# Performance work log

Hardware: AMD Instinct MI355X
Metric: run time of the kernel (lower is better)

Reference implementation:

```python
import jax, jax.numpy as jnp
import numpy as np

E = 1024   # emb_dim
H = 1024   # hidden_size
L = 2      # num_layers
V = 50257  # vocab_size
S = 2048   # encoder input length
T = 2048   # decoder target length


def setup_inputs() -> dict:
    key = jax.random.key(0)
    ks = jax.random.split(key, 16)
    s = 0.02  # init scale
    f32 = jnp.float32
    return {
        "inputs": jax.random.randint(ks[0], (1, S), 0, V),
        "outputs": jax.random.randint(ks[1], (1, T), 0, V),
        "sos": 1,
        "enc_emb": jax.random.normal(ks[2], (V, E), f32) * s,
        "dec_emb": jax.random.normal(ks[3], (V, E), f32) * s,
        # Stacked LSTM weights; layer-0 input dim == E == H so layers stack.
        "enc_Wih": jax.random.normal(ks[4], (L, 4 * H, H), f32) * s,
        "enc_Whh": jax.random.normal(ks[5], (L, 4 * H, H), f32) * s,
        "enc_bih": jax.random.normal(ks[6], (L, 4 * H), f32) * s,
        "enc_bhh": jax.random.normal(ks[7], (L, 4 * H), f32) * s,
        "dec_Wih": jax.random.normal(ks[8], (L, 4 * H, H), f32) * s,
        "dec_Whh": jax.random.normal(ks[9], (L, 4 * H, H), f32) * s,
        "dec_bih": jax.random.normal(ks[10], (L, 4 * H), f32) * s,
        "dec_bhh": jax.random.normal(ks[11], (L, 4 * H), f32) * s,
        "lin_W": jax.random.normal(ks[12], (V, H), f32) * s,
        "lin_b": jax.random.normal(ks[13], (V,), f32) * s,
    }


def _run_stack(xs, Wih, Whh, bih, bhh, h0, c0):
    # xs: [S, E]; Wih/Whh: [L, 4H, H]; h0/c0: [L, H]
    # PyTorch LSTM gate order: i, f, g, o.
    h_fin, c_fin = [], []
    for l in range(Wih.shape[0]):
        Wi, Wh, bi, bh = Wih[l], Whh[l], bih[l], bhh[l]

        def step(carry, x, Wi=Wi, Wh=Wh, bi=bi, bh=bh):
            h, c = carry
            g = Wi @ x + bi + Wh @ h + bh           # [4H]
            i, f, gg, o = jnp.split(g, 4)
            c = jax.nn.sigmoid(f) * c + jax.nn.sigmoid(i) * jnp.tanh(gg)
            h = jax.nn.sigmoid(o) * jnp.tanh(c)
            return (h, c), h

        (h, c), xs = jax.lax.scan(step, (h0[l], c0[l]), xs)
        h_fin.append(h)
        c_fin.append(c)
    return xs, jnp.stack(h_fin), jnp.stack(c_fin)


def reference(inputs, outputs, sos, enc_emb, dec_emb,
              enc_Wih, enc_Whh, enc_bih, enc_bhh,
              dec_Wih, dec_Whh, dec_bih, dec_bhh,
              lin_W, lin_b):
    # Encoder over the source sequence (batch == 1, squeezed away).
    x = enc_emb[inputs[0]]                       # [S, E]
    z = jnp.zeros((L, H), dtype=x.dtype)
    _, hN, cN = _run_stack(x, enc_Wih, enc_Whh, enc_bih, enc_bhh, z, z)
    # Full teacher forcing: decoder inputs are [sos, outputs[:, :-1]].
    dec_tokens = jnp.concatenate(
        [jnp.array([sos], dtype=outputs.dtype), outputs[0, :-1]])
    y = dec_emb[dec_tokens]                      # [T, E]
    dec_out, _, _ = _run_stack(y, dec_Wih, dec_Whh, dec_bih, dec_bhh, hN, cN)
    logits = dec_out @ lin_W.T + lin_b           # [T, V]
    return logits
```

## Files before the change

### kernel.cpp

```cpp
#include <hip/hip_runtime.h>
#include <hip/hip_bf16.h>
#include <math.h>

#define S_LEN 2048
#define T_LEN 2048
#define HID   1024
#define GATES 4096
#define VOCAB 50257
#define SPINCAP 262144

typedef unsigned int u32;
typedef unsigned long long ull;
typedef u32 u32x4 __attribute__((ext_vector_type(4)));
typedef float f32x4 __attribute__((ext_vector_type(4)));

__device__ __forceinline__ float fsig_(float x)  { return 1.0f / (1.0f + __expf(-x)); }
__device__ __forceinline__ float ftanh_(float x) { float e = __expf(2.0f * x); return 1.0f - 2.0f / (e + 1.0f); }

__device__ __forceinline__ u32x4 cload16(const ull* p) {
  u32x4 v;
  asm volatile("global_load_dwordx4 %0, %1, off sc0 sc1\n\ts_waitcnt vmcnt(0)"
               : "=v"(v) : "v"(p) : "memory");
  return v;
}

__device__ __forceinline__ u32x4 pollslots(const ull* p, u32 want) {
  u32x4 v = cload16(p);
  int n = 0;
  while (v.y < want || v.w < want) {
    if (++n > SPINCAP) break;
    v = cload16(p);
  }
  return v;
}

__global__ void zero_f4(float4* __restrict__ p, size_t n4) {
  size_t i = (size_t)blockIdx.x * blockDim.x + threadIdx.x;
  size_t stride = (size_t)gridDim.x * blockDim.x;
  for (; i < n4; i += stride) p[i] = make_float4(0.f, 0.f, 0.f, 0.f);
}

__global__ void build_dec_tokens(const int* __restrict__ outputs, const int* __restrict__ sos,
                                 int* __restrict__ toks, int T) {
  int t = blockIdx.x * blockDim.x + threadIdx.x;
  if (t < T) toks[t] = (t == 0) ? sos[0] : outputs[t - 1];
}

__global__ __launch_bounds__(256) void gemm_xwt(
    const float* __restrict__ X, const float* __restrict__ W,
    const float* __restrict__ b1,
    float* __restrict__ C, int M, int N, int K)
{
  __shared__ float Xs[16][68];
  __shared__ float Ws[16][68];
  const int tid = threadIdx.x;
  const int tx = tid & 15;
  const int ty = tid >> 4;
  const int m0 = blockIdx.y * 64;
  const int n0 = blockIdx.x * 64;
  const int lr = tid >> 2;
  const int lc = (tid & 3) * 4;
  float acc[4][4] = {{0.f}};

  for (int k0 = 0; k0 < K; k0 += 16) {
    float4 xv = *(const float4*)(X + (size_t)(m0 + lr) * K + k0 + lc);
    float4 wv = make_float4(0.f, 0.f, 0.f, 0.f);
    int wr = n0 + lr;
    if (wr < N) wv = *(const float4*)(W + (size_t)wr * K + k0 + lc);
    __syncthreads();
    Xs[lc + 0][lr] = xv.x; Xs[lc + 1][lr] = xv.y; Xs[lc + 2][lr] = xv.z; Xs[lc + 3][lr] = xv.w;
    Ws[lc + 0][lr] = wv.x; Ws[lc + 1][lr] = wv.y; Ws[lc + 2][lr] = wv.z; Ws[lc + 3][lr] = wv.w;
    __syncthreads();
#pragma unroll
    for (int kk = 0; kk < 16; ++kk) {
      float4 a = *(const float4*)&Xs[kk][ty * 4];
      float4 b = *(const float4*)&Ws[kk][tx * 4];
      float av[4] = {a.x, a.y, a.z, a.w};
      float bv[4] = {b.x, b.y, b.z, b.w};
#pragma unroll
      for (int i = 0; i < 4; ++i)
#pragma unroll
        for (int j = 0; j < 4; ++j)
          acc[i][j] = fmaf(av[i], bv[j], acc[i][j]);
    }
  }
#pragma unroll
  for (int i = 0; i < 4; ++i) {
    int m = m0 + ty * 4 + i;
#pragma unroll
    for (int j = 0; j < 4; ++j) {
      int n = n0 + tx * 4 + j;
      if (n < N) C[(size_t)m * N + n] = acc[i][j] + (b1 ? b1[n] : 0.f);
    }
  }
}

__global__ __launch_bounds__(512, 1) void lstm2(
    const float* __restrict__ emb,  const int* __restrict__ toks,
    const float* __restrict__ Wi0,  const float* __restrict__ Wh0,
    const float* __restrict__ bi0,  const float* __restrict__ bh0,
    const float* __restrict__ Wi1,  const float* __restrict__ Wh1,
    const float* __restrict__ bi1,  const float* __restrict__ bh1,
    const float* __restrict__ h00,  const float* __restrict__ c00,
    const float* __restrict__ h01,  const float* __restrict__ c01,
    ull* __restrict__ s0, ull* __restrict__ s1,
    float* __restrict__ hf0, float* __restrict__ cf0,
    float* __restrict__ hf1, float* __restrict__ cf1,
    float* __restrict__ dec_out, int T)
{
  const int tid = threadIdx.x;
  const int wg  = blockIdx.x;
  const bool isL0 = (wg < 128);
  const int wgl = isL0 ? wg : wg - 128;

  const int lane16 = tid & 15;
  const int rloc = tid >> 4;
  const int jloc = rloc & 7;
  const int gate = rloc >> 3;
  const int grow = gate * HID + wgl * 8 + jloc;

  __shared__ float lds_x[2][HID];
  __shared__ float lds_h[HID];
  __shared__ float lds_g[32];
  __shared__ float lds_c[8];

  const float* Wi = isL0 ? Wi0 : Wi1;
  const float* Wh = isL0 ? Wh0 : Wh1;
  const float breg = (isL0 ? (bi0[grow] + bh0[grow]) : (bi1[grow] + bh1[grow]));

  f32x4 Wir[16], Whr[16];
  {
    const f32x4* wi = (const f32x4*)(Wi + (size_t)grow * HID);
    const f32x4* wh = (const f32x4*)(Wh + (size_t)grow * HID);
#pragma unroll
    for (int i = 0; i < 16; ++i) {
      Wir[i] = wi[lane16 + i * 16];
      Whr[i] = wh[lane16 + i * 16];
    }
  }
#pragma unroll
  for (int i = 0; i < 16; ++i)
    asm volatile("" : "+v"(Wir[i]), "+v"(Whr[i]));

  {
    const float* hini = isL0 ? h00 : h01;
    const float* cini = isL0 ? c00 : c01;
    if (tid < 8) lds_c[tid] = cini[wgl * 8 + tid];
    if (tid < 256) ((float4*)lds_h)[tid] = ((const float4*)hini)[tid];
    if (isL0 && tid < 256) {
      int tok = toks[0];
      ((float4*)lds_x[0])[tid] = ((const float4*)(emb + (size_t)tok * HID))[tid];
    }
  }
  __syncthreads();

  ull* s_mine = isL0 ? s0 : s1;

  for (int t = 0; t < T; ++t) {
    const int cur = t & 1;

    if (isL0) {
      if (t > 0) {
        const ull* ph = s0 + (size_t)(t - 1) * HID + 2 * tid;
        u32x4 v = pollslots(ph, (u32)t);
        lds_h[2 * tid]     = __uint_as_float(v.x);
        lds_h[2 * tid + 1] = __uint_as_float(v.z);
      }
    } else {
      {
        const ull* px = s0 + (size_t)t * HID + 2 * tid;
        u32x4 v = pollslots(px, (u32)(t + 1));
        lds_x[0][2 * tid]     = __uint_as_float(v.x);
        lds_x[0][2 * tid + 1] = __uint_as_float(v.z);
      }
      if (t > 0) {
        const ull* ph = s1 + (size_t)(t - 1) * HID + 2 * tid;
        u32x4 v = pollslots(ph, (u32)t);
        lds_h[2 * tid]     = __uint_as_float(v.x);
        lds_h[2 * tid + 1] = __uint_as_float(v.z);
      }
    }
    __syncthreads();

    if (isL0 && tid < 256 && t + 1 < T) {
      int tok = toks[t + 1];
      ((float4*)lds_x[cur ^ 1])[tid] = ((const float4*)(emb + (size_t)tok * HID))[tid];
    }

    const float* xbuf = isL0 ? lds_x[cur] : lds_x[0];
    float p0 = 0.f, p1 = 0.f, p2 = 0.f, p3 = 0.f;
#pragma unroll
    for (int i = 0; i < 16; ++i) {
      const float4 xv = *(const float4*)&xbuf[(lane16 << 2) + (i << 6)];
      p0 = fmaf(Wir[i].x, xv.x, p0);
      p1 = fmaf(Wir[i].y, xv.y, p1);
      p2 = fmaf(Wir[i].z, xv.z, p2);
      p3 = fmaf(Wir[i].w, xv.w, p3);
    }
#pragma unroll
    for (int i = 0; i < 16; ++i) {
      const float4 hv = *(const float4*)&lds_h[(lane16 << 2) + (i << 6)];
      p0 = fmaf(Whr[i].x, hv.x, p0);
      p1 = fmaf(Whr[i].y, hv.y, p1);
      p2 = fmaf(Whr[i].z, hv.z, p2);
      p3 = fmaf(Whr[i].w, hv.w, p3);
    }
    float sum = (p0 + p1) + (p2 + p3);
    sum += __shfl_xor(sum, 1);
    sum += __shfl_xor(sum, 2);
    sum += __shfl_xor(sum, 4);
    sum += __shfl_xor(sum, 8);
    if (lane16 == 0) lds_g[rloc] = sum + breg;
    __syncthreads();

    if (tid < 8) {
      const float gi = lds_g[tid];
      const float gf = lds_g[8 + tid];
      const float gg = lds_g[16 + tid];
      const float go = lds_g[24 + tid];
      const float c = fsig_(gf) * lds_c[tid] + fsig_(gi) * ftanh_(gg);
      const float h = fsig_(go) * ftanh_(c);
      lds_c[tid] = c;
      const int col = wgl * 8 + tid;
      const ull pk = ((ull)(u32)(t + 1) << 32) | (ull)__float_as_uint(h);
      __hip_atomic_store(&s_mine[(size_t)t * HID + col], pk,
                         __ATOMIC_RELAXED, __HIP_MEMORY_SCOPE_AGENT);
      if (!isL0 && dec_out) dec_out[(size_t)t * HID + col] = h;
      if (t == T - 1) {
        if (isL0) { if (hf0) hf0[col] = h; if (cf0) cf0[col] = c; }
        else      { if (hf1) hf1[col] = h; if (cf1) cf1[col] = c; }
      }
    }
  }
}

extern "C" void kernel_launch(void* const* d_in, const int* in_sizes, int n_in,
                              void* d_out, int out_size, void* d_ws, size_t ws_size,
                              hipStream_t stream) {
  const int*   inputs  = (const int*)d_in[0];
  const int*   outputs = (const int*)d_in[1];
  const int*   sos     = (const int*)d_in[2];
  const float* enc_emb = (const float*)d_in[3];
  const float* dec_emb = (const float*)d_in[4];
  const float* enc_Wih = (const float*)d_in[5];
  const float* enc_Whh = (const float*)d_in[6];
  const float* enc_bih = (const float*)d_in[7];
  const float* enc_bhh = (const float*)d_in[8];
  const float* dec_Wih = (const float*)d_in[9];
  const float* dec_Whh = (const float*)d_in[10];
  const float* dec_bih = (const float*)d_in[11];
  const float* dec_bhh = (const float*)d_in[12];
  const float* lin_W   = (const float*)d_in[13];
  const float* lin_b   = (const float*)d_in[14];

  float* out = (float*)d_out;
  ull* s0e = (ull*)d_out;
  ull* s1e = s0e + 2097152;
  ull* s0d = s1e + 2097152;
  ull* s1d = s0d + 2097152;

  char* ws = (char*)d_ws;
  float* zerosv = (float*)(ws + 0);
  float* hf0    = (float*)(ws + 4096);
  float* cf0    = (float*)(ws + 8192);
  float* hf1    = (float*)(ws + 12288);
  float* cf1    = (float*)(ws + 16384);
  int*   dtoks  = (int*)(ws + 20480);
  float* B2     = (float*)(ws + ((size_t)1 << 20));

  const size_t WOFF = (size_t)GATES * HID;

  zero_f4<<<2048, 256, 0, stream>>>((float4*)d_out, 4194304);
  zero_f4<<<1, 256, 0, stream>>>((float4*)zerosv, 256);
  build_dec_tokens<<<8, 256, 0, stream>>>(outputs, sos, dtoks, T_LEN);

  lstm2<<<256, 512, 0, stream>>>(
      enc_emb, inputs,
      enc_Wih, enc_Whh, enc_bih, enc_bhh,
      enc_Wih + WOFF, enc_Whh + WOFF, enc_bih + GATES, enc_bhh + GATES,
      zerosv, zerosv, zerosv, zerosv,
      s0e, s1e, hf0, cf0, hf1, cf1, nullptr, S_LEN);

  lstm2<<<256, 512, 0, stream>>>(
      dec_emb, dtoks,
      dec_Wih, dec_Whh, dec_bih, dec_bhh,
      dec_Wih + WOFF, dec_Whh + WOFF, dec_bih + GATES, dec_bhh + GATES,
      hf0, cf0, hf1, cf1,
      s0d, s1d, nullptr, nullptr, nullptr, nullptr, B2, T_LEN);

  dim3 gemmV_grid((VOCAB + 63) / 64, T_LEN / 64);
  gemm_xwt<<<gemmV_grid, 256, 0, stream>>>(B2, lin_W, lin_b, out, T_LEN, VOCAB, HID);
}
```

Before: 15.93 ms.

## Use split-bf16 MFMA for logits GEMM and pipeline LSTM spin-polling

Replaces the FP32 scalar FMA logits GEMM with a bf16 MFMA kernel. It emulates fp32 precision by splitting activations and weights into hi/lo bf16 parts and running three MFMAs per tile, with activations pre-split by a new kernel. The LSTM inter-block polling now uses a software-pipelined inline-asm loop over two 8-byte slots, the spin cap is removed, and the register-pinning asm barriers on the weight registers are dropped. The aim is to cut the dominant vocab projection cost and the per-step sync latency. The trade-off is some accuracy from the split-bf16 approximation and the risk of an unbounded hang if a slot is never written.

```diff
diff --git a/kernel.cpp b/kernel.cpp
--- a/kernel.cpp
+++ b/kernel.cpp
@@ -7,31 +7,63 @@
 #define HID   1024
 #define GATES 4096
 #define VOCAB 50257
-#define SPINCAP 262144
 
 typedef unsigned int u32;
+typedef unsigned short u16;
 typedef unsigned long long ull;
 typedef u32 u32x4 __attribute__((ext_vector_type(4)));
 typedef float f32x4 __attribute__((ext_vector_type(4)));
+typedef short s16x8 __attribute__((ext_vector_type(8)));
 
 __device__ __forceinline__ float fsig_(float x)  { return 1.0f / (1.0f + __expf(-x)); }
 __device__ __forceinline__ float ftanh_(float x) { float e = __expf(2.0f * x); return 1.0f - 2.0f / (e + 1.0f); }
 
-__device__ __forceinline__ u32x4 cload16(const ull* p) {
-  u32x4 v;
-  asm volatile("global_load_dwordx4 %0, %1, off sc0 sc1\n\ts_waitcnt vmcnt(0)"
-               : "=v"(v) : "v"(p) : "memory");
-  return v;
-}
-
-__device__ __forceinline__ u32x4 pollslots(const ull* p, u32 want) {
-  u32x4 v = cload16(p);
-  int n = 0;
-  while (v.y < want || v.w < want) {
-    if (++n > SPINCAP) break;
-    v = cload16(p);
-  }
-  return v;
+__device__ __forceinline__ u32 bf16rne(float x) {
+  u32 u = __float_as_uint(x);
+  return (u + 0x7FFFu + ((u >> 16) & 1u)) >> 16;
+}
+__device__ __forceinline__ float bf16tof(u32 b) { return __uint_as_float(b << 16); }
+
+__device__ __forceinline__ void pollpipe2(const ull* p0, const ull* p1, u32 want,
+                                          ull& ra, ull& rb) {
+  ull r0a, r0b, r1a, r1b, stmp;
+  u32 par;
+  const ull wantv = ((ull)want) << 32;
+  asm volatile(
+    "s_waitcnt vmcnt(0)\n\t"
+    "global_load_dwordx2 %[r0a], %[p0], off sc0 sc1\n\t"
+    "global_load_dwordx2 %[r0b], %[p1], off sc0 sc1\n\t"
+    "1:\n\t"
+    "global_load_dwordx2 %[r1a], %[p0], off sc0 sc1\n\t"
+    "global_load_dwordx2 %[r1b], %[p1], off sc0 sc1\n\t"
+    "s_waitcnt vmcnt(2)\n\t"
+    "v_cmp_lt_u64 vcc, %[r0a], %[wv]\n\t"
+    "s_mov_b64 %[st], vcc\n\t"
+    "v_cmp_lt_u64 vcc, %[r0b], %[wv]\n\t"
+    "s_or_b64 vcc, vcc, %[st]\n\t"
+    "s_cbranch_vccz 2f\n\t"
+    "global_load_dwordx2 %[r0a], %[p0], off sc0 sc1\n\t"
+    "global_load_dwordx2 %[r0b], %[p1], off sc0 sc1\n\t"
+    "s_waitcnt vmcnt(2)\n\t"
+    "v_cmp_lt_u64 vcc, %[r1a], %[wv]\n\t"
+    "s_mov_b64 %[st], vcc\n\t"
+    "v_cmp_lt_u64 vcc, %[r1b], %[wv]\n\t"
+    "s_or_b64 vcc, vcc, %[st]\n\t"
+    "s_cbranch_vccz 3f\n\t"
+    "s_branch 1b\n\t"
+    "2:\n\t"
+    "s_mov_b32 %[par], 0\n\t"
+    "s_branch 4f\n\t"
+    "3:\n\t"
+    "s_mov_b32 %[par], 1\n\t"
+    "4:\n\t"
+    "s_waitcnt vmcnt(0)"
+    : [r0a]"=&v"(r0a), [r0b]"=&v"(r0b), [r1a]"=&v"(r1a), [r1b]"=&v"(r1b),
+      [st]"=&s"(stmp), [par]"=&s"(par)
+    : [p0]"v"(p0), [p1]"v"(p1), [wv]"v"(wantv)
+    : "vcc", "memory");
+  ra = par ? r1a : r0a;
+  rb = par ? r1b : r0b;
 }
 
 __global__ void zero_f4(float4* __restrict__ p, size_t n4) {
@@ -46,53 +78,89 @@
   if (t < T) toks[t] = (t == 0) ? sos[0] : outputs[t - 1];
 }
 
-__global__ __launch_bounds__(256) void gemm_xwt(
-    const float* __restrict__ X, const float* __restrict__ W,
-    const float* __restrict__ b1,
+__global__ void xsplit(const float* __restrict__ x, u16* __restrict__ hi,
+                       u16* __restrict__ lo, int n) {
+  int i = blockIdx.x * 256 + threadIdx.x;
+  if (i < n) {
+    float v = x[i];
+    u32 h = bf16rne(v);
+    hi[i] = (u16)h;
+    lo[i] = (u16)bf16rne(v - bf16tof(h));
+  }
+}
+
+__global__ __launch_bounds__(256) void gemm_logits(
+    const u16* __restrict__ Xhi, const u16* __restrict__ Xlo,
+    const float* __restrict__ W, const float* __restrict__ b,
     float* __restrict__ C, int M, int N, int K)
 {
-  __shared__ float Xs[16][68];
-  __shared__ float Ws[16][68];
+  __shared__ u16 Bhi[64][40];
+  __shared__ u16 Blo[64][40];
   const int tid = threadIdx.x;
-  const int tx = tid & 15;
-  const int ty = tid >> 4;
-  const int m0 = blockIdx.y * 64;
-  const int n0 = blockIdx.x * 64;
-  const int lr = tid >> 2;
-  const int lc = (tid & 3) * 4;
-  float acc[4][4] = {{0.f}};
-
-  for (int k0 = 0; k0 < K; k0 += 16) {
-    float4 xv = *(const float4*)(X + (size_t)(m0 + lr) * K + k0 + lc);
-    float4 wv = make_float4(0.f, 0.f, 0.f, 0.f);
-    int wr = n0 + lr;
-    if (wr < N) wv = *(const float4*)(W + (size_t)wr * K + k0 + lc);
+  const int wv  = tid >> 6;
+  const int l   = tid & 63;
+  const int l15 = l & 15;
+  const int kro = (l >> 4) * 8;
+  const int m0  = blockIdx.y * 128;
+  const int n0  = blockIdx.x * 64;
+  const int srow = tid >> 2;
+  const int skp  = (tid & 3) * 8;
+
+  f32x4 acc[2][4] = {};
+
+  for (int k0 = 0; k0 < K; k0 += 32) {
+    float w[8] = {0.f};
+    {
+      int wr = n0 + srow;
+      if (wr < N) {
+        const float4 a = *(const float4*)(W + (size_t)wr * K + k0 + skp);
+        const float4 c = *(const float4*)(W + (size_t)wr * K + k0 + skp + 4);
+        w[0] = a.x; w[1] = a.y; w[2] = a.z; w[3] = a.w;
+        w[4] = c.x; w[5] = c.y; w[6] = c.z; w[7] = c.w;
+      }
+    }
     __syncthreads();
-    Xs[lc + 0][lr] = xv.x; Xs[lc + 1][lr] = xv.y; Xs[lc + 2][lr] = xv.z; Xs[lc + 3][lr] = xv.w;
-    Ws[lc + 0][lr] = wv.x; Ws[lc + 1][lr] = wv.y; Ws[lc + 2][lr] = wv.z; Ws[lc + 3][lr] = wv.w;
+#pragma unroll
+    for (int e = 0; e < 8; ++e) {
+      u32 h = bf16rne(w[e]);
+      Bhi[srow][skp + e] = (u16)h;
+      Blo[srow][skp + e] = (u16)bf16rne(w[e] - bf16tof(h));
+    }
     __syncthreads();
-#pragma unroll
-    for (int kk = 0; kk < 16; ++kk) {
-      float4 a = *(const float4*)&Xs[kk][ty * 4];
-      float4 b = *(const float4*)&Ws[kk][tx * 4];
-      float av[4] = {a.x, a.y, a.z, a.w};
-      float bv[4] = {b.x, b.y, b.z, b.w};
-#pragma unroll
-      for (int i = 0; i < 4; ++i)
-#pragma unroll
-        for (int j = 0; j < 4; ++j)
-          acc[i][j] = fmaf(av[i], bv[j], acc[i][j]);
-    }
-  }
-#pragma unroll
-  for (int i = 0; i < 4; ++i) {
-    int m = m0 + ty * 4 + i;
-#pragma unroll
-    for (int j = 0; j < 4; ++j) {
-      int n = n0 + tx * 4 + j;
-      if (n < N) C[(size_t)m * N + n] = acc[i][j] + (b1 ? b1[n] : 0.f);
-    }
-  }
+
+    const size_t xoff0 = (size_t)(m0 + wv * 32 + l15) * K + k0 + kro;
+    const size_t xoff1 = xoff0 + (size_t)16 * K;
+    s16x8 ah0 = *(const s16x8*)(Xhi + xoff0);
+    s16x8 al0 = *(const s16x8*)(Xlo + xoff0);
+    s16x8 ah1 = *(const s16x8*)(Xhi + xoff1);
+    s16x8 al1 = *(const s16x8*)(Xlo + xoff1);
+#pragma unroll
+    for (int tn = 0; tn < 4; ++tn) {
+      s16x8 bh = *(const s16x8*)&Bhi[tn * 16 + l15][kro];
+      s16x8 bl = *(const s16x8*)&Blo[tn * 16 + l15][kro];
+      acc[0][tn] = __builtin_amdgcn_mfma_f32_16x16x32_bf16(ah0, bh, acc[0][tn], 0, 0, 0);
+      acc[0][tn] = __builtin_amdgcn_mfma_f32_16x16x32_bf16(al0, bh, acc[0][tn], 0, 0, 0);
+      acc[0][tn] = __builtin_amdgcn_mfma_f32_16x16x32_bf16(ah0, bl, acc[0][tn], 0, 0, 0);
+      acc[1][tn] = __builtin_amdgcn_mfma_f32_16x16x32_bf16(ah1, bh, acc[1][tn], 0, 0, 0);
+      acc[1][tn] = __builtin_amdgcn_mfma_f32_16x16x32_bf16(al1, bh, acc[1][tn], 0, 0, 0);
+      acc[1][tn] = __builtin_amdgcn_mfma_f32_16x16x32_bf16(ah1, bl, acc[1][tn], 0, 0, 0);
+    }
+  }
+
+#pragma unroll
+  for (int tm = 0; tm < 2; ++tm)
+#pragma unroll
+    for (int tn = 0; tn < 4; ++tn) {
+      int n = n0 + tn * 16 + l15;
+      if (n < N) {
+        float bias = b[n];
+#pragma unroll
+        for (int r = 0; r < 4; ++r) {
+          int m = m0 + wv * 32 + tm * 16 + (l >> 4) * 4 + r;
+          C[(size_t)m * N + n] = acc[tm][tn][r] + bias;
+        }
+      }
+    }
 }
 
 __global__ __launch_bounds__(512, 1) void lstm2(
@@ -138,9 +206,6 @@
       Whr[i] = wh[lane16 + i * 16];
     }
   }
-#pragma unroll
-  for (int i = 0; i < 16; ++i)
-    asm volatile("" : "+v"(Wir[i]), "+v"(Whr[i]));
 
   {
     const float* hini = isL0 ? h00 : h01;
@@ -161,23 +226,26 @@
 
     if (isL0) {
       if (t > 0) {
-        const ull* ph = s0 + (size_t)(t - 1) * HID + 2 * tid;
-        u32x4 v = pollslots(ph, (u32)t);
-        lds_h[2 * tid]     = __uint_as_float(v.x);
-        lds_h[2 * tid + 1] = __uint_as_float(v.z);
+        ull va, vb;
+        pollpipe2(s0 + (size_t)(t - 1) * HID + 2 * tid,
+                  s0 + (size_t)(t - 1) * HID + 2 * tid + 1, (u32)t, va, vb);
+        lds_h[2 * tid]     = __uint_as_float((u32)va);
+        lds_h[2 * tid + 1] = __uint_as_float((u32)vb);
       }
     } else {
       {
-        const ull* px = s0 + (size_t)t * HID + 2 * tid;
-        u32x4 v = pollslots(px, (u32)(t + 1));
-        lds_x[0][2 * tid]     = __uint_as_float(v.x);
-        lds_x[0][2 * tid + 1] = __uint_as_float(v.z);
+        ull va, vb;
+        pollpipe2(s0 + (size_t)t * HID + 2 * tid,
+                  s0 + (size_t)t * HID + 2 * tid + 1, (u32)(t + 1), va, vb);
+        lds_x[0][2 * tid]     = __uint_as_float((u32)va);
+        lds_x[0][2 * tid + 1] = __uint_as_float((u32)vb);
       }
       if (t > 0) {
-        const ull* ph = s1 + (size_t)(t - 1) * HID + 2 * tid;
-        u32x4 v = pollslots(ph, (u32)t);
-        lds_h[2 * tid]     = __uint_as_float(v.x);
-        lds_h[2 * tid + 1] = __uint_as_float(v.z);
+        ull va, vb;
+        pollpipe2(s1 + (size_t)(t - 1) * HID + 2 * tid,
+                  s1 + (size_t)(t - 1) * HID + 2 * tid + 1, (u32)t, va, vb);
+        lds_h[2 * tid]     = __uint_as_float((u32)va);
+        lds_h[2 * tid + 1] = __uint_as_float((u32)vb);
       }
     }
     __syncthreads();
@@ -267,6 +335,8 @@
   float* cf1    = (float*)(ws + 16384);
   int*   dtoks  = (int*)(ws + 20480);
   float* B2     = (float*)(ws + ((size_t)1 << 20));
+  u16*   Xhi    = (u16*)(ws + ((size_t)10 << 20));
+  u16*   Xlo    = (u16*)(ws + ((size_t)15 << 20));
 
   const size_t WOFF = (size_t)GATES * HID;
 
@@ -288,6 +358,8 @@
       hf0, cf0, hf1, cf1,
       s0d, s1d, nullptr, nullptr, nullptr, nullptr, B2, T_LEN);
 
-  dim3 gemmV_grid((VOCAB + 63) / 64, T_LEN / 64);
-  gemm_xwt<<<gemmV_grid, 256, 0, stream>>>(B2, lin_W, lin_b, out, T_LEN, VOCAB, HID);
-}
+  xsplit<<<(T_LEN * HID + 255) / 256, 256, 0, stream>>>(B2, Xhi, Xlo, T_LEN * HID);
+  dim3 gemmV_grid((VOCAB + 63) / 64, T_LEN / 128);
+  gemm_logits<<<gemmV_grid, 256, 0, stream>>>(Xhi, Xlo, lin_W, lin_b, out,
+                                              T_LEN, VOCAB, HID);
+}
```

Result: faster. 12.87 ms (-19.2%).
